# Performance work log

Hardware: AMD Instinct MI355X
Metric: run time of the kernel (lower is better)

The kernel has to match this reference:

```python
import jax, jax.numpy as jnp
import numpy as np

BATCH = 8
IMG = 224
PATCH = 16
IN_CH = 8
D_MODEL = 768
DEPTH = 4
D_INNER = 2 * D_MODEL          # 1536
D_STATE = 16
DT_RANK = D_MODEL // 16        # 48
D_CONV = 4
NUM_CLASSES = 1000
EPS = 1e-5


def setup_inputs() -> dict:
    key = jax.random.key(0)
    ks = jax.random.split(key, 16)
    g = lambda i, shape, s=0.02: jax.random.normal(ks[i], shape, jnp.float32) * s
    L = DEPTH
    inp = {}
    inp['x'] = jax.random.normal(ks[0], (BATCH, IN_CH, IMG, IMG), jnp.float32)
    # patch embed: Conv3d(1, D, (1,p,p)) == shared 2D conv applied to every channel
    inp['patch_w'] = g(1, (D_MODEL, PATCH, PATCH))
    inp['patch_b'] = jnp.zeros((D_MODEL,), jnp.float32)
    inp['channel_embed'] = g(2, (IN_CH, D_MODEL))
    # per-block params (stacked over depth)
    inp['norm_w'] = jnp.ones((L, D_MODEL), jnp.float32)
    inp['norm_b'] = jnp.zeros((L, D_MODEL), jnp.float32)
    inp['in_proj_w'] = g(3, (L, 2 * D_INNER, D_MODEL))
    inp['conv_w'] = g(4, (L, D_INNER, D_CONV), 0.1)
    inp['conv_b'] = jnp.zeros((L, D_INNER), jnp.float32)
    inp['x_proj_w'] = g(5, (L, DT_RANK + 2 * D_STATE, D_INNER))
    inp['dt_proj_w'] = g(6, (L, D_INNER, DT_RANK), 0.1)
    inp['dt_proj_b'] = jnp.full((L, D_INNER), -4.6, jnp.float32)  # softplus^-1(0.01)
    inp['A_log'] = jnp.tile(jnp.log(jnp.arange(1, D_STATE + 1, dtype=jnp.float32)), (L, D_INNER, 1))
    inp['D_param'] = jnp.ones((L, D_INNER), jnp.float32)
    inp['ssm_norm_w'] = jnp.ones((L, D_INNER), jnp.float32)
    inp['ssm_norm_b'] = jnp.zeros((L, D_INNER), jnp.float32)
    inp['out_proj_w'] = g(7, (L, D_MODEL, D_INNER), 0.02 / np.sqrt(L))
    # final norm + classification head
    inp['norm_f_w'] = jnp.ones((D_MODEL,), jnp.float32)
    inp['norm_f_b'] = jnp.zeros((D_MODEL,), jnp.float32)
    inp['head_w'] = g(8, (NUM_CLASSES, D_MODEL))
    inp['head_b'] = jnp.zeros((NUM_CLASSES,), jnp.float32)
    return inp


def _ln(x, w, b):
    mu = x.mean(-1, keepdims=True)
    var = ((x - mu) ** 2).mean(-1, keepdims=True)
    return (x - mu) * jax.lax.rsqrt(var + EPS) * w + b


def _silu(x):
    return x * jax.nn.sigmoid(x)


def _mamba(h, ipw, cw, cb, xpw, dtw, dtb, Alog, Dp, snw, snb, opw):
    # h: [B, L, D_MODEL]
    B, Lseq, _ = h.shape
    xz = jnp.einsum('bld,ed->ble', h, ipw)               # [B, L, 2*di]
    x, z = jnp.split(xz, 2, axis=-1)
    # causal depthwise conv1d along L (kernel D_CONV)
    xp = jnp.pad(x, ((0, 0), (D_CONV - 1, 0), (0, 0)))
    xc = cb + sum(xp[:, k:k + Lseq, :] * cw[:, k] for k in range(D_CONV))
    x = _silu(xc)
    dbc = jnp.einsum('bld,ed->ble', x, xpw)              # [B, L, dt_rank+2N]
    dt_r = dbc[..., :DT_RANK]
    Bm = dbc[..., DT_RANK:DT_RANK + D_STATE]
    Cm = dbc[..., DT_RANK + D_STATE:]
    dt = jax.nn.softplus(jnp.einsum('blr,dr->bld', dt_r, dtw) + dtb)  # [B, L, di]
    A = -jnp.exp(Alog)                                    # [di, N]

    def step(hstate, t):
        dt_t, B_t, C_t, x_t = t                           # [B,di],[B,N],[B,N],[B,di]
        dA = jnp.exp(dt_t[..., None] * A)                 # [B, di, N]
        hstate = dA * hstate + (dt_t * x_t)[..., None] * B_t[:, None, :]
        y = jnp.einsum('bdn,bn->bd', hstate, C_t)
        return hstate, y

    h0 = jnp.zeros((B, D_INNER, D_STATE), x.dtype)
    xs = (dt.transpose(1, 0, 2), Bm.transpose(1, 0, 2),
          Cm.transpose(1, 0, 2), x.transpose(1, 0, 2))
    _, ys = jax.lax.scan(step, h0, xs)                    # [L, B, di]
    y = ys.transpose(1, 0, 2) + Dp * x
    y = _ln(y, snw, snb)                                  # norm-after-SSM
    y = y * _silu(z)
    return jnp.einsum('ble,de->bld', y, opw)


def reference(x, patch_w, patch_b, channel_embed, norm_w, norm_b, in_proj_w,
              conv_w, conv_b, x_proj_w, dt_proj_w, dt_proj_b, A_log, D_param,
              ssm_norm_w, ssm_norm_b, out_proj_w, norm_f_w, norm_f_b,
              head_w, head_b):
    B, C, H, W = x.shape
    hg, wg = H // PATCH, W // PATCH
    # shared-filter patch embed per channel: [B,C,hg,wg,D]
    xp = x.reshape(B, C, hg, PATCH, wg, PATCH)
    emb = jnp.einsum('bchpwq,dpq->bchwd', xp, patch_w) + patch_b
    emb = emb + channel_embed[None, :, None, None, :]
    # Channel-First scan order -> token order (h, w, C): [B, hg*wg*C, D]
    tok = emb.transpose(0, 2, 3, 1, 4).reshape(B, hg * wg * C, D_MODEL)

    hidden, residual = tok, None
    for i in range(DEPTH):
        residual = hidden if residual is None else residual + hidden
        hn = _ln(residual, norm_w[i], norm_b[i])
        hidden = _mamba(hn, in_proj_w[i], conv_w[i], conv_b[i], x_proj_w[i],
                        dt_proj_w[i], dt_proj_b[i], A_log[i], D_param[i],
                        ssm_norm_w[i], ssm_norm_b[i], out_proj_w[i])
    residual = residual + hidden
    hf = _ln(residual, norm_f_w, norm_f_b)
    pooled = hf.mean(axis=1)                              # mean pooling head
    return pooled @ head_w.T + head_b
```

## Files before the change

### kernel.cpp

```cpp
#include <hip/hip_runtime.h>
#include <hip/hip_bf16.h>

typedef __hip_bfloat16 bf16;
typedef __attribute__((ext_vector_type(8))) short short8;
typedef __attribute__((ext_vector_type(4))) float float4v;

#define BATCH 8
#define SEQ   1568
#define M_TOK (BATCH*SEQ)
#define DM    768
#define DI    1536
#define DS    16
#define DTR   48
#define NCLS  1000
#define LAYERS 4
#define CHUNK 112
#define NCH   14

__device__ __forceinline__ float b2f(bf16 v){ return __bfloat162float(v); }
__device__ __forceinline__ bf16  f2b(float v){ return __float2bfloat16(v); }
__device__ __forceinline__ float us2f(unsigned short u){
    unsigned v = ((unsigned)u) << 16; float f; __builtin_memcpy(&f, &v, 4); return f;
}
__device__ __forceinline__ void gload_lds16(const void* g, void* l){
    __builtin_amdgcn_global_load_lds(
        (const __attribute__((address_space(1))) void*)g,
        (__attribute__((address_space(3))) void*)l, 16, 0, 0);
}
template<int CTRL>
__device__ __forceinline__ float dpp_add(float p){
    int pi; __builtin_memcpy(&pi, &p, 4);
    int mi = __builtin_amdgcn_update_dpp(pi, pi, CTRL, 0xF, 0xF, false);
    float m; __builtin_memcpy(&m, &mi, 4);
    return p + m;
}

__global__ void detect_dtype(const unsigned short* __restrict__ probe, unsigned* __restrict__ flag)
{
    if (threadIdx.x == 0 && blockIdx.x == 0) flag[0] = (probe[0] == 0) ? 1u : 0u;
}

__global__ __launch_bounds__(256)
void to_bf16(const unsigned* __restrict__ flag, const void* __restrict__ src,
             bf16* __restrict__ dst, int n)
{
    int i = blockIdx.x*256 + threadIdx.x;
    if (i >= n) return;
    dst[i] = flag[0] ? f2b(((const float*)src)[i]) : ((const bf16*)src)[i];
}

__global__ __launch_bounds__(256)
void to_f32(const unsigned* __restrict__ flag, const void* __restrict__ src,
            float* __restrict__ dst, int n)
{
    int i = blockIdx.x*256 + threadIdx.x;
    if (i >= n) return;
    dst[i] = flag[0] ? ((const float*)src)[i] : b2f(((const bf16*)src)[i]);
}

__global__ __launch_bounds__(256)
void gather_patches(const bf16* __restrict__ x, bf16* __restrict__ Ap, int b0)
{
    size_t idx = (size_t)blockIdx.x*256 + threadIdx.x;
    int i = (int)(idx & 255);
    int m = (int)(idx >> 8);
    int b = b0 + m / SEQ, s = m % SEQ;
    int hw = s >> 3, c = s & 7;
    int h = hw / 14, w = hw % 14;
    int p = i >> 4, q = i & 15;
    Ap[idx] = x[(((size_t)(b*8 + c)*224) + h*16 + p)*224 + w*16 + q];
}

__global__ __launch_bounds__(256)
void gemm_mfma(const bf16* __restrict__ A, int lda,
               const bf16* __restrict__ W, int ldw,
               float* __restrict__ Cf, bf16* __restrict__ Cb, int ldc,
               const float* __restrict__ bias, const float* __restrict__ chan,
               int M, int N, int K, int epi)
{
    __shared__ short As[128*40];
    __shared__ short Bs[128*40];
    int tid  = threadIdx.x;
    int m0   = blockIdx.x*128, n0 = blockIdx.y*128;
    int lane = tid & 63, wv = tid >> 6;
    int wm = (wv >> 1)*64, wn = (wv & 1)*64;
    int l15 = lane & 15, quad = lane >> 4;

    float4v acc[4][4];
    #pragma unroll
    for (int i = 0; i < 4; ++i)
        #pragma unroll
        for (int j = 0; j < 4; ++j) acc[i][j] = (float4v){0.f,0.f,0.f,0.f};

    const short8 zv8 = {0,0,0,0,0,0,0,0};
    for (int k0 = 0; k0 < K; k0 += 32) {
        #pragma unroll
        for (int u = 0; u < 2; ++u) {
            int c   = tid*2 + u;
            int row = c >> 2, ch = c & 3;
            bool kok = (k0 + ch*8 + 8) <= K;
            short8 va = (kok && m0 + row < M)
                ? *(const short8*)((const short*)A + (size_t)(m0+row)*lda + k0 + ch*8) : zv8;
            *(short8*)(As + row*40 + ch*8) = va;
            short8 vb = (kok && n0 + row < N)
                ? *(const short8*)((const short*)W + (size_t)(n0+row)*ldw + k0 + ch*8) : zv8;
            *(short8*)(Bs + row*40 + ch*8) = vb;
        }
        __syncthreads();
        short8 av[4], bv[4];
        #pragma unroll
        for (int i = 0; i < 4; ++i) av[i] = *(const short8*)(As + (wm + i*16 + l15)*40 + quad*8);
        #pragma unroll
        for (int j = 0; j < 4; ++j) bv[j] = *(const short8*)(Bs + (wn + j*16 + l15)*40 + quad*8);
        #pragma unroll
        for (int i = 0; i < 4; ++i)
            #pragma unroll
            for (int j = 0; j < 4; ++j)
                acc[i][j] = __builtin_amdgcn_mfma_f32_16x16x32_bf16(av[i], bv[j], acc[i][j], 0, 0, 0);
        __syncthreads();
    }

    #pragma unroll
    for (int i = 0; i < 4; ++i) {
        #pragma unroll
        for (int j = 0; j < 4; ++j) {
            int gn = n0 + wn + j*16 + l15;
            if (gn >= N) continue;
            #pragma unroll
            for (int r = 0; r < 4; ++r) {
                int gm = m0 + wm + i*16 + quad*4 + r;
                if (gm >= M) continue;
                float v = acc[i][j][r];
                size_t off = (size_t)gm*ldc + gn;
                if (epi == 0)      Cb[off] = f2b(v);
                else if (epi == 1) {
                    v += bias[gn];
                    v = (v > 20.f) ? v : log1pf(__expf(v));
                    Cb[off] = f2b(v);
                }
                else if (epi == 2) Cf[off] += v;
                else               Cf[off] = v + bias[gn] + chan[(size_t)(gm & 7)*N + gn];
            }
        }
    }
}

__global__ __launch_bounds__(256)
void gemm_mfma_fast(const bf16* __restrict__ A, int lda,
                    const bf16* __restrict__ W, int ldw,
                    float* __restrict__ Cf, bf16* __restrict__ Cb, int ldc,
                    const float* __restrict__ bias, const float* __restrict__ chan,
                    int N, int K, int epi)
{
    __shared__ short As[128*32];
    __shared__ short Bs[128*32];
    int tid  = threadIdx.x;
    int m0   = blockIdx.x*128, n0 = blockIdx.y*128;
    int lane = tid & 63, wv = tid >> 6;
    int wm = (wv >> 1)*64, wn = (wv & 1)*64;
    int l15 = lane & 15, quad = lane >> 4;

    int srow = (lane >> 2);
    int skof = (lane & 3) * 8;

    float4v acc[4][4];
    #pragma unroll
    for (int i = 0; i < 4; ++i)
        #pragma unroll
        for (int j = 0; j < 4; ++j) acc[i][j] = (float4v){0.f,0.f,0.f,0.f};

    const short* Ab = (const short*)A;
    const short* Wb = (const short*)W;

    for (int k0 = 0; k0 < K; k0 += 32) {
        #pragma unroll
        for (int u = 0; u < 2; ++u) {
            int c = wv*2 + u;
            int row = c*16 + srow;
            gload_lds16(Ab + (size_t)(m0+row)*lda + k0 + skof, As + c*512);
            gload_lds16(Wb + (size_t)(n0+row)*ldw + k0 + skof, Bs + c*512);
        }
        __syncthreads();
        short8 av[4], bv[4];
        #pragma unroll
        for (int i = 0; i < 4; ++i) av[i] = *(const short8*)(As + (wm + i*16 + l15)*32 + quad*8);
        #pragma unroll
        for (int j = 0; j < 4; ++j) bv[j] = *(const short8*)(Bs + (wn + j*16 + l15)*32 + quad*8);
        #pragma unroll
        for (int i = 0; i < 4; ++i)
            #pragma unroll
            for (int j = 0; j < 4; ++j)
                acc[i][j] = __builtin_amdgcn_mfma_f32_16x16x32_bf16(av[i], bv[j], acc[i][j], 0, 0, 0);
        __syncthreads();
    }

    #pragma unroll
    for (int i = 0; i < 4; ++i) {
        #pragma unroll
        for (int j = 0; j < 4; ++j) {
            int gn = n0 + wn + j*16 + l15;
            #pragma unroll
            for (int r = 0; r < 4; ++r) {
                int gm = m0 + wm + i*16 + quad*4 + r;
                float v = acc[i][j][r];
                size_t off = (size_t)gm*ldc + gn;
                if (epi == 0)      Cb[off] = f2b(v);
                else if (epi == 1) {
                    v += bias[gn];
                    v = (v > 20.f) ? v : log1pf(__expf(v));
                    Cb[off] = f2b(v);
                }
                else if (epi == 2) Cf[off] += v;
                else               Cf[off] = v + bias[gn] + chan[(size_t)(gm & 7)*N + gn];
            }
        }
    }
}

__global__ __launch_bounds__(256)
void ln768(const float* __restrict__ X, const float* __restrict__ w,
           const float* __restrict__ bb, bf16* __restrict__ out)
{
    __shared__ float red[8];
    size_t t = blockIdx.x;
    const float* x = X + t*DM;
    float v[3]; float s = 0.f, s2 = 0.f;
    #pragma unroll
    for (int r = 0; r < 3; ++r) {
        v[r] = x[threadIdx.x + 256*r];
        s += v[r]; s2 += v[r]*v[r];
    }
    #pragma unroll
    for (int o = 32; o; o >>= 1) { s += __shfl_down(s, o, 64); s2 += __shfl_down(s2, o, 64); }
    if ((threadIdx.x & 63) == 0) { red[threadIdx.x >> 6] = s; red[(threadIdx.x >> 6) + 4] = s2; }
    __syncthreads();
    s  = red[0]+red[1]+red[2]+red[3];
    s2 = red[4]+red[5]+red[6]+red[7];
    float mu  = s * (1.f/DM);
    float inv = rsqrtf(fmaxf(s2*(1.f/DM) - mu*mu, 0.f) + 1e-5f);
    #pragma unroll
    for (int r = 0; r < 3; ++r) {
        int i = threadIdx.x + 256*r;
        out[t*DM + i] = f2b((v[r]-mu)*inv*w[i] + bb[i]);
    }
}

__global__ __launch_bounds__(256)
void conv_silu(const bf16* __restrict__ xh, const float* __restrict__ cw,
               const float* __restrict__ cb, bf16* __restrict__ xc)
{
    size_t idx = (size_t)blockIdx.x*256 + threadIdx.x;
    int dv = (int)(idx % (DI/8));
    int m  = (int)(idx / (DI/8));
    int b = m / SEQ, t = m % SEQ;
    int d = dv*8;

    float4v cwq[8];
    #pragma unroll
    for (int j = 0; j < 8; ++j) cwq[j] = *(const float4v*)(cw + (size_t)(d+j)*4);

    float acc[8];
    #pragma unroll
    for (int j = 0; j < 8; ++j) acc[j] = cb[d+j];

    #pragma unroll
    for (int k = 0; k < 4; ++k) {
        int tt = t + k - 3;
        if (tt >= 0) {
            short8 v = *(const short8*)((const short*)xh + (size_t)(b*SEQ + tt)*DI + d);
            #pragma unroll
            for (int j = 0; j < 8; ++j)
                acc[j] += us2f((unsigned short)v[j]) * cwq[j][k];
        }
    }
    short8 o;
    #pragma unroll
    for (int j = 0; j < 8; ++j) {
        float sig = 1.f/(1.f + __expf(-acc[j]));
        bf16 r = f2b(acc[j]*sig);
        unsigned short u; __builtin_memcpy(&u, &r, 2); o[j] = (short)u;
    }
    *(short8*)((short*)xc + idx*8) = o;
}


__global__ __launch_bounds__(256)
void scan_pass1(const bf16* __restrict__ dt, const bf16* __restrict__ x,
                const bf16* __restrict__ dbc, const float* __restrict__ Alog,
                float* __restrict__ hend, float* __restrict__ Pprod, int nin)
{
    __shared__ float dtsT[2][16][20], xsT[2][16][20], BshT[2][16][20];
    int c  = blockIdx.x / nin;
    int r  = blockIdx.x % nin;
    int b  = r / 96;
    int d0 = (r % 96) * 16;
    int tid = threadIdx.x;
    int s  = tid & 15;
    int dl = tid >> 4;
    int d  = d0 + dl;

    float A2 = -__expf(Alog[(size_t)d*DS + s]) * 1.44269504f;
    float h = 0.f, sdt = 0.f;

    int wv   = tid >> 6;
    int lane = tid & 63;
    int st = lane >> 2;
    int sd = (lane & 3) * 4;
    int tbase = c * CHUNK;
    const int NT = CHUNK/16;

    const unsigned short* sp0 = nullptr;
    size_t rstride = 0;
    float* dst0 = nullptr;
    {
        size_t rb = (size_t)(b*SEQ + st);
        if (wv == 0)      { sp0 = (const unsigned short*)dt  + rb*DI + d0 + sd; rstride = DI; dst0 = &dtsT[0][0][0]; }
        else if (wv == 1) { sp0 = (const unsigned short*)x   + rb*DI + d0 + sd; rstride = DI; dst0 = &xsT[0][0][0]; }
        else if (wv == 2) { sp0 = (const unsigned short*)dbc + rb*80 + DTR + sd; rstride = 80; dst0 = &BshT[0][0][0]; }
    }
    const size_t bufstride = 16*20;

    ushort4 vr;
    if (wv < 3) {
        vr = *(const ushort4*)(sp0 + (size_t)tbase*rstride);
        dst0[(sd+0)*20 + st] = us2f(vr.x);
        dst0[(sd+1)*20 + st] = us2f(vr.y);
        dst0[(sd+2)*20 + st] = us2f(vr.z);
        dst0[(sd+3)*20 + st] = us2f(vr.w);
        vr = *(const ushort4*)(sp0 + (size_t)(tbase+16)*rstride);
    }
    __syncthreads();

    for (int t = 0; t < NT; ++t) {
        int cur = t & 1;
        if (wv < 3) {
            if (t+1 < NT) {
                float* dstp = dst0 + (size_t)(cur^1)*bufstride;
                dstp[(sd+0)*20 + st] = us2f(vr.x);
                dstp[(sd+1)*20 + st] = us2f(vr.y);
                dstp[(sd+2)*20 + st] = us2f(vr.z);
                dstp[(sd+3)*20 + st] = us2f(vr.w);
            }
            if (t+2 < NT)
                vr = *(const ushort4*)(sp0 + (size_t)(tbase+(t+2)*16)*rstride);
        }
        #pragma unroll
        for (int jj = 0; jj < 16; jj += 4) {
            float4v dtq = *(const float4v*)&dtsT[cur][dl][jj];
            float4v xq  = *(const float4v*)&xsT [cur][dl][jj];
            float4v Bq  = *(const float4v*)&BshT[cur][s][jj];
            #pragma unroll
            for (int k = 0; k < 4; ++k) {
                float dtv = dtq[k];
                h = exp2f(dtv*A2)*h + (dtv*xq[k])*Bq[k];
                sdt += dtv;
            }
        }
        __syncthreads();
    }
    size_t o = ((size_t)c*nin + r)*256 + tid;
    hend [o] = h;
    Pprod[o] = exp2f(A2*sdt);
}

__global__ __launch_bounds__(256)
void scan_mid(const float* __restrict__ hend, const float* __restrict__ Pprod,
              float* __restrict__ hstart, int nin)
{
    int r = blockIdx.x, tid = threadIdx.x;
    float h = 0.f;
    hstart[(size_t)r*256 + tid] = 0.f;
    for (int c = 1; c < NCH; ++c) {
        size_t p = ((size_t)(c-1)*nin + r)*256 + tid;
        h = Pprod[p]*h + hend[p];
        hstart[((size_t)c*nin + r)*256 + tid] = h;
    }
}

__global__ __launch_bounds__(256)
void scan_pass2(const bf16* __restrict__ dt, const bf16* __restrict__ x,
                const bf16* __restrict__ dbc, const float* __restrict__ Alog,
                const float* __restrict__ Dpar, const float* __restrict__ hstart,
                bf16* __restrict__ y, int nin)
{
    __shared__ float dtsT[2][16][20], xsT[2][16][20], BshT[2][16][20], CshT[2][16][20];
    __shared__ bf16  ys[16][16];
    int c  = blockIdx.x / nin;
    int r  = blockIdx.x % nin;
    int b  = r / 96;
    int d0 = (r % 96) * 16;
    int tid = threadIdx.x;
    int s  = tid & 15;
    int dl = tid >> 4;
    int d  = d0 + dl;

    float A2 = -__expf(Alog[(size_t)d*DS + s]) * 1.44269504f;
    float Dv = Dpar[d];
    float h  = hstart[((size_t)c*nin + r)*256 + tid];

    int wv   = tid >> 6;
    int lane = tid & 63;
    int st = lane >> 2;
    int sd = (lane & 3) * 4;
    int tbase = c * CHUNK;
    const int NT = CHUNK/16;

    const unsigned short* sp0;
    size_t rstride;
    float* dst0;
    {
        size_t rb = (size_t)(b*SEQ + st);
        if (wv == 0)      { sp0 = (const unsigned short*)dt  + rb*DI + d0 + sd;       rstride = DI; dst0 = &dtsT[0][0][0]; }
        else if (wv == 1) { sp0 = (const unsigned short*)x   + rb*DI + d0 + sd;       rstride = DI; dst0 = &xsT[0][0][0]; }
        else if (wv == 2) { sp0 = (const unsigned short*)dbc + rb*80 + DTR + sd;      rstride = 80; dst0 = &BshT[0][0][0]; }
        else              { sp0 = (const unsigned short*)dbc + rb*80 + DTR + DS + sd; rstride = 80; dst0 = &CshT[0][0][0]; }
    }
    const size_t bufstride = 16*20;

    ushort4 vr = *(const ushort4*)(sp0 + (size_t)tbase*rstride);
    dst0[(sd+0)*20 + st] = us2f(vr.x);
    dst0[(sd+1)*20 + st] = us2f(vr.y);
    dst0[(sd+2)*20 + st] = us2f(vr.z);
    dst0[(sd+3)*20 + st] = us2f(vr.w);
    vr = *(const ushort4*)(sp0 + (size_t)(tbase+16)*rstride);
    __syncthreads();

    for (int t = 0; t < NT; ++t) {
        int cur = t & 1;
        if (t+1 < NT) {
            float* dstp = dst0 + (size_t)(cur^1)*bufstride;
            dstp[(sd+0)*20 + st] = us2f(vr.x);
            dstp[(sd+1)*20 + st] = us2f(vr.y);
            dstp[(sd+2)*20 + st] = us2f(vr.z);
            dstp[(sd+3)*20 + st] = us2f(vr.w);
        }
        if (t+2 < NT)
            vr = *(const ushort4*)(sp0 + (size_t)(tbase+(t+2)*16)*rstride);

        #pragma unroll
        for (int jj = 0; jj < 16; jj += 4) {
            float4v dtq = *(const float4v*)&dtsT[cur][dl][jj];
            float4v xq  = *(const float4v*)&xsT [cur][dl][jj];
            float4v Bq  = *(const float4v*)&BshT[cur][s][jj];
            float4v Cq  = *(const float4v*)&CshT[cur][s][jj];
            #pragma unroll
            for (int k = 0; k < 4; ++k) {
                float dtv = dtq[k];
                float xv  = xq[k];
                h = exp2f(dtv*A2)*h + (dtv*xv)*Bq[k];
                float p = h*Cq[k];
                p = dpp_add<0xB1>(p);
                p = dpp_add<0x4E>(p);
                p = dpp_add<0x124>(p);
                p = dpp_add<0x128>(p);
                if (s == 0) ys[jj+k][dl] = f2b(p + Dv*xv);
            }
        }
        __syncthreads();
        if (wv == 0) {
            size_t rowm = (size_t)(b*SEQ + tbase + t*16 + st);
            ushort4 vy = *(const ushort4*)((const unsigned short*)&ys[st][0] + sd);
            *(ushort4*)((unsigned short*)y + rowm*DI + d0 + sd) = vy;
        }
        __syncthreads();
    }
}

__global__ __launch_bounds__(256)
void gate_ln(const bf16* __restrict__ y, const bf16* __restrict__ z,
             const float* __restrict__ w, const float* __restrict__ bb,
             bf16* __restrict__ out)
{
    __shared__ float red[8];
    size_t t = blockIdx.x;
    const bf16* yy = y + t*DI;
    const bf16* zz = z + t*DI;
    float v[6]; float s = 0.f, s2 = 0.f;
    #pragma unroll
    for (int r = 0; r < 6; ++r) {
        v[r] = b2f(yy[threadIdx.x + 256*r]);
        s += v[r]; s2 += v[r]*v[r];
    }
    #pragma unroll
    for (int o = 32; o; o >>= 1) { s += __shfl_down(s, o, 64); s2 += __shfl_down(s2, o, 64); }
    if ((threadIdx.x & 63) == 0) { red[threadIdx.x >> 6] = s; red[(threadIdx.x >> 6) + 4] = s2; }
    __syncthreads();
    s  = red[0]+red[1]+red[2]+red[3];
    s2 = red[4]+red[5]+red[6]+red[7];
    float mu  = s * (1.f/DI);
    float inv = rsqrtf(fmaxf(s2*(1.f/DI) - mu*mu, 0.f) + 1e-5f);
    #pragma unroll
    for (int r = 0; r < 6; ++r) {
        int i = threadIdx.x + 256*r;
        float zv = b2f(zz[i]);
        float sig = 1.f/(1.f + __expf(-zv));
        out[t*DI + i] = f2b(((v[r]-mu)*inv*w[i] + bb[i]) * (zv*sig));
    }
}

__global__ __launch_bounds__(256)
void pool_kernel(const bf16* __restrict__ hf, float* __restrict__ pooled)
{
    int idx = blockIdx.x*256 + threadIdx.x;
    int b = idx / DM, dm = idx % DM;
    const bf16* p = hf + (size_t)b*SEQ*DM + dm;
    float s = 0.f;
    for (int t = 0; t < SEQ; ++t) s += b2f(p[(size_t)t*DM]);
    pooled[idx] = s * (1.f/SEQ);
}

__global__ __launch_bounds__(256)
void head_kernel(const unsigned* __restrict__ flag,
                 const float* __restrict__ pooled, const bf16* __restrict__ hw,
                 const float* __restrict__ hb, void* __restrict__ out)
{
    int idx = blockIdx.x*256 + threadIdx.x;
    if (idx >= BATCH*NCLS) return;
    int b = idx & 7, n = idx >> 3;
    const float* p = pooled + b*DM;
    const unsigned short* w = (const unsigned short*)hw + (size_t)n*DM;
    float acc = hb[n];
    for (int k = 0; k < DM; k += 4) {
        ushort4 wv = *(const ushort4*)(w + k);
        acc += p[k]*us2f(wv.x) + p[k+1]*us2f(wv.y) + p[k+2]*us2f(wv.z) + p[k+3]*us2f(wv.w);
    }
    int o = b*NCLS + n;
    if (flag[0]) ((float*)out)[o] = acc;
    else         ((bf16*)out)[o]  = f2b(acc);
}

extern "C" void kernel_launch(void* const* d_in, const int* in_sizes, int n_in,
                              void* d_out, int out_size, void* d_ws, size_t ws_size,
                              hipStream_t stream)
{
    (void)n_in; (void)out_size;
    dim3 blk(256);

    const bool is_f32[21] = { false, false, true, true, true, true, false, true, true,
                              false, false, true,  true, true, true, true, false,
                              true,  true,  false, true };

    size_t off = 0;
    auto carve = [&](size_t bytes) -> void* {
        void* q = (char*)d_ws + off;
        off += (bytes + 255) & ~(size_t)255;
        return q;
    };

    unsigned* flag = (unsigned*)carve(256);
    void* canon[21];
    for (int i = 0; i < 21; ++i)
        canon[i] = carve((size_t)in_sizes[i] * (is_f32[i] ? 4 : 2));

    float* residual = (float*)carve((size_t)M_TOK*DM*4);
    bf16*  hn       = (bf16*) carve((size_t)M_TOK*DM*2);
    float* pooled   = (float*)carve((size_t)BATCH*DM*4);

    const size_t scanbuf1 = (size_t)NCH*96*256*4;
    const size_t inner1 = 4*(((size_t)SEQ*DI*2 + 255) & ~(size_t)255)
                          + (((size_t)SEQ*80*2 + 255) & ~(size_t)255)
                          + 3*((scanbuf1 + 255) & ~(size_t)255);
    int g = 8;
    while (g > 1 && off + (size_t)g*inner1 > ws_size) g >>= 1;

    bf16* xh  = (bf16*)carve((size_t)g*SEQ*DI*2);
    bf16* zh  = (bf16*)carve((size_t)g*SEQ*DI*2);
    bf16* xc  = (bf16*)carve((size_t)g*SEQ*DI*2);
    bf16* dtb = (bf16*)carve((size_t)g*SEQ*DI*2);
    bf16* dbc = (bf16*)carve((size_t)g*SEQ*80*2);
    float* hend   = (float*)carve((size_t)g*scanbuf1);
    float* Pprod  = (float*)carve((size_t)g*scanbuf1);
    float* hstart = (float*)carve((size_t)g*scanbuf1);
    bf16* Ap    = xh;
    bf16* ybuf  = xh;
    bf16* gated = dtb;

    detect_dtype<<<1, 64, 0, stream>>>((const unsigned short*)d_in[4], flag);
    for (int i = 0; i < 21; ++i) {
        int n = in_sizes[i];
        int gr = (n + 255)/256;
        if (is_f32[i]) to_f32 <<<gr, blk, 0, stream>>>(flag, d_in[i], (float*)canon[i], n);
        else           to_bf16<<<gr, blk, 0, stream>>>(flag, d_in[i], (bf16*) canon[i], n);
    }

    const bf16*  xin   = (const bf16*) canon[0];
    const bf16*  pw    = (const bf16*) canon[1];
    const float* pb    = (const float*)canon[2];
    const float* chan  = (const float*)canon[3];
    const float* nw    = (const float*)canon[4];
    const float* nb    = (const float*)canon[5];
    const bf16*  ipw   = (const bf16*) canon[6];
    const float* cw    = (const float*)canon[7];
    const float* cb    = (const float*)canon[8];
    const bf16*  xpw   = (const bf16*) canon[9];
    const bf16*  dtw   = (const bf16*) canon[10];
    const float* dtbia = (const float*)canon[11];
    const float* Alog  = (const float*)canon[12];
    const float* Dpar  = (const float*)canon[13];
    const float* snw   = (const float*)canon[14];
    const float* snb   = (const float*)canon[15];
    const bf16*  opw   = (const bf16*) canon[16];
    const float* nfw   = (const float*)canon[17];
    const float* nfb   = (const float*)canon[18];
    const bf16*  hw    = (const bf16*) canon[19];
    const float* hb    = (const float*)canon[20];

    const int MG  = g*SEQ;
    const int GXm = (MG + 127)/128;
    const int nin = g*96;

    auto launch_gemm = [&](const bf16* A, int lda, const bf16* W, int ldw,
                           float* Cf, bf16* Cb, int ldc,
                           const float* bias, const float* chan_,
                           int M, int N, int K, int epi) {
        dim3 gr((M + 127)/128, (N + 127)/128);
        if ((M & 127) == 0 && (N & 127) == 0 && (K & 31) == 0)
            gemm_mfma_fast<<<gr, blk, 0, stream>>>(A, lda, W, ldw, Cf, Cb, ldc,
                                                   bias, chan_, N, K, epi);
        else
            gemm_mfma<<<gr, blk, 0, stream>>>(A, lda, W, ldw, Cf, Cb, ldc,
                                              bias, chan_, M, N, K, epi);
    };

    for (int b0 = 0; b0 < BATCH; b0 += g) {
        gather_patches<<<MG, blk, 0, stream>>>(xin, Ap, b0);
        launch_gemm(Ap, 256, pw, 256,
                    residual + (size_t)b0*SEQ*DM, nullptr, DM,
                    pb, chan, MG, DM, 256, 3);
    }

    for (int l = 0; l < LAYERS; ++l) {
        ln768<<<M_TOK, blk, 0, stream>>>(residual, nw + l*DM, nb + l*DM, hn);
        for (int b0 = 0; b0 < BATCH; b0 += g) {
            const bf16* hng = hn + (size_t)b0*SEQ*DM;
            launch_gemm(hng, DM, ipw + (size_t)l*2*DI*DM, DM,
                        nullptr, xh, DI, nullptr, nullptr, MG, DI, DM, 0);
            launch_gemm(hng, DM, ipw + (size_t)l*2*DI*DM + (size_t)DI*DM, DM,
                        nullptr, zh, DI, nullptr, nullptr, MG, DI, DM, 0);
            conv_silu<<<(MG*(DI/8))/256, blk, 0, stream>>>(xh, cw + (size_t)l*DI*4, cb + l*DI, xc);
            launch_gemm(xc, DI, xpw + (size_t)l*80*DI, DI,
                        nullptr, dbc, 80, nullptr, nullptr, MG, 80, DI, 0);
            launch_gemm(dbc, 80, dtw + (size_t)l*DI*DTR, DTR,
                        nullptr, dtb, DI, dtbia + l*DI, nullptr, MG, DI, DTR, 1);
            scan_pass1<<<(NCH-1)*nin, blk, 0, stream>>>(dtb, xc, dbc,
                                                        Alog + (size_t)l*DI*DS,
                                                        hend, Pprod, nin);
            scan_mid<<<nin, blk, 0, stream>>>(hend, Pprod, hstart, nin);
            scan_pass2<<<NCH*nin, blk, 0, stream>>>(dtb, xc, dbc,
                                                    Alog + (size_t)l*DI*DS,
                                                    Dpar + l*DI, hstart, ybuf, nin);
            gate_ln<<<MG, blk, 0, stream>>>(ybuf, zh, snw + l*DI, snb + l*DI, gated);
            launch_gemm(gated, DI, opw + (size_t)l*DM*DI, DI,
                        residual + (size_t)b0*SEQ*DM, nullptr, DM,
                        nullptr, nullptr, MG, DM, DI, 2);
        }
    }

    ln768<<<M_TOK, blk, 0, stream>>>(residual, nfw, nfb, hn);
    pool_kernel<<<(BATCH*DM)/256, blk, 0, stream>>>(hn, pooled);
    head_kernel<<<(BATCH*NCLS + 255)/256, blk, 0, stream>>>(flag, pooled, hw, hb, d_out);
}
```

Measured before the change: 3.957 ms.

## Give each scan thread four states and widen blocks to 64 channels

The selective-scan kernels are remapped so each thread owns four SSM states for one channel instead of one, and each block covers 64 channels instead of 16. dt and x are now loaded once per channel rather than per state, LDS staging is spread across all waves, and the C reduction needs two DPP steps instead of four. The output write uses all threads. This cuts redundant LDS reads and shuffle work per state, in exchange for more registers per thread and a quarter as many blocks.

```diff
diff --git a/kernel.cpp b/kernel.cpp
--- a/kernel.cpp
+++ b/kernel.cpp
@@ -287,93 +287,94 @@
 __global__ __launch_bounds__(256)
 void scan_pass1(const bf16* __restrict__ dt, const bf16* __restrict__ x,
                 const bf16* __restrict__ dbc, const float* __restrict__ Alog,
-                float* __restrict__ hend, float* __restrict__ Pprod, int nin)
-{
-    __shared__ float dtsT[2][16][20], xsT[2][16][20], BshT[2][16][20];
-    int c  = blockIdx.x / nin;
-    int r  = blockIdx.x % nin;
-    int b  = r / 96;
-    int d0 = (r % 96) * 16;
+                float* __restrict__ hend, float* __restrict__ Pprod, int nin2)
+{
+    __shared__ float dtT[2][64][20], xT[2][64][20];
+    __shared__ float BsT[2][16][16];
+    int c  = blockIdx.x / nin2;
+    int r  = blockIdx.x % nin2;
+    int b  = r / 24;
+    int d0 = (r % 24) * 64;
     int tid = threadIdx.x;
-    int s  = tid & 15;
-    int dl = tid >> 4;
+    int sq = tid & 3;
+    int dl = tid >> 2;
     int d  = d0 + dl;
 
-    float A2 = -__expf(Alog[(size_t)d*DS + s]) * 1.44269504f;
-    float h = 0.f, sdt = 0.f;
-
-    int wv   = tid >> 6;
-    int lane = tid & 63;
-    int st = lane >> 2;
-    int sd = (lane & 3) * 4;
+    float4v Aq = *(const float4v*)(Alog + (size_t)d*DS + sq*4);
+    float A2[4], h[4];
+    #pragma unroll
+    for (int k = 0; k < 4; ++k) { A2[k] = -__expf(Aq[k]) * 1.44269504f; h[k] = 0.f; }
+    float sdt = 0.f;
+
+    int js = tid >> 4, dg = tid & 15;
+    bool doB = tid < 64;
+    int j2 = tid >> 2;
+
+    const unsigned short* pdt = (const unsigned short*)dt + ((size_t)b*SEQ + js)*DI + d0 + dg*4;
+    const unsigned short* px  = (const unsigned short*)x  + ((size_t)b*SEQ + js)*DI + d0 + dg*4;
+    const unsigned short* pbc = (const unsigned short*)dbc + ((size_t)b*SEQ + (j2 & 15))*80 + DTR + sq*4;
     int tbase = c * CHUNK;
     const int NT = CHUNK/16;
 
-    const unsigned short* sp0 = nullptr;
-    size_t rstride = 0;
-    float* dst0 = nullptr;
-    {
-        size_t rb = (size_t)(b*SEQ + st);
-        if (wv == 0)      { sp0 = (const unsigned short*)dt  + rb*DI + d0 + sd; rstride = DI; dst0 = &dtsT[0][0][0]; }
-        else if (wv == 1) { sp0 = (const unsigned short*)x   + rb*DI + d0 + sd; rstride = DI; dst0 = &xsT[0][0][0]; }
-        else if (wv == 2) { sp0 = (const unsigned short*)dbc + rb*80 + DTR + sd; rstride = 80; dst0 = &BshT[0][0][0]; }
-    }
-    const size_t bufstride = 16*20;
-
-    ushort4 vr;
-    if (wv < 3) {
-        vr = *(const ushort4*)(sp0 + (size_t)tbase*rstride);
-        dst0[(sd+0)*20 + st] = us2f(vr.x);
-        dst0[(sd+1)*20 + st] = us2f(vr.y);
-        dst0[(sd+2)*20 + st] = us2f(vr.z);
-        dst0[(sd+3)*20 + st] = us2f(vr.w);
-        vr = *(const ushort4*)(sp0 + (size_t)(tbase+16)*rstride);
-    }
+    ushort4 vdt, vx, vbc;
+    auto stage = [&](int buf){
+        dtT[buf][dg*4+0][js] = us2f(vdt.x); dtT[buf][dg*4+1][js] = us2f(vdt.y);
+        dtT[buf][dg*4+2][js] = us2f(vdt.z); dtT[buf][dg*4+3][js] = us2f(vdt.w);
+        xT [buf][dg*4+0][js] = us2f(vx.x);  xT [buf][dg*4+1][js] = us2f(vx.y);
+        xT [buf][dg*4+2][js] = us2f(vx.z);  xT [buf][dg*4+3][js] = us2f(vx.w);
+        if (doB)
+            *(float4v*)&BsT[buf][j2][sq*4] =
+                (float4v){us2f(vbc.x), us2f(vbc.y), us2f(vbc.z), us2f(vbc.w)};
+    };
+    auto fetch = [&](int T){
+        vdt = *(const ushort4*)(pdt + (size_t)(tbase + T*16)*DI);
+        vx  = *(const ushort4*)(px  + (size_t)(tbase + T*16)*DI);
+        if (doB) vbc = *(const ushort4*)(pbc + (size_t)(tbase + T*16)*80);
+    };
+
+    fetch(0); stage(0); fetch(1);
     __syncthreads();
 
     for (int t = 0; t < NT; ++t) {
         int cur = t & 1;
-        if (wv < 3) {
-            if (t+1 < NT) {
-                float* dstp = dst0 + (size_t)(cur^1)*bufstride;
-                dstp[(sd+0)*20 + st] = us2f(vr.x);
-                dstp[(sd+1)*20 + st] = us2f(vr.y);
-                dstp[(sd+2)*20 + st] = us2f(vr.z);
-                dstp[(sd+3)*20 + st] = us2f(vr.w);
-            }
-            if (t+2 < NT)
-                vr = *(const ushort4*)(sp0 + (size_t)(tbase+(t+2)*16)*rstride);
-        }
+        if (t+1 < NT) stage(cur^1);
+        if (t+2 < NT) fetch(t+2);
         #pragma unroll
         for (int jj = 0; jj < 16; jj += 4) {
-            float4v dtq = *(const float4v*)&dtsT[cur][dl][jj];
-            float4v xq  = *(const float4v*)&xsT [cur][dl][jj];
-            float4v Bq  = *(const float4v*)&BshT[cur][s][jj];
+            float4v dtq = *(const float4v*)&dtT[cur][dl][jj];
+            float4v xq  = *(const float4v*)&xT [cur][dl][jj];
             #pragma unroll
-            for (int k = 0; k < 4; ++k) {
-                float dtv = dtq[k];
-                h = exp2f(dtv*A2)*h + (dtv*xq[k])*Bq[k];
+            for (int k2 = 0; k2 < 4; ++k2) {
+                float dtv = dtq[k2];
+                float dtx = dtv * xq[k2];
+                float4v Bq = *(const float4v*)&BsT[cur][jj+k2][sq*4];
+                #pragma unroll
+                for (int k = 0; k < 4; ++k)
+                    h[k] = exp2f(dtv*A2[k])*h[k] + dtx*Bq[k];
                 sdt += dtv;
             }
         }
         __syncthreads();
     }
-    size_t o = ((size_t)c*nin + r)*256 + tid;
-    hend [o] = h;
-    Pprod[o] = exp2f(A2*sdt);
+    size_t o = (((size_t)c*nin2 + r)*256 + tid)*4;
+    *(float4v*)(hend + o) = (float4v){h[0], h[1], h[2], h[3]};
+    *(float4v*)(Pprod + o) = (float4v){exp2f(A2[0]*sdt), exp2f(A2[1]*sdt),
+                                       exp2f(A2[2]*sdt), exp2f(A2[3]*sdt)};
 }
 
 __global__ __launch_bounds__(256)
 void scan_mid(const float* __restrict__ hend, const float* __restrict__ Pprod,
-              float* __restrict__ hstart, int nin)
+              float* __restrict__ hstart, int nin2)
 {
     int r = blockIdx.x, tid = threadIdx.x;
-    float h = 0.f;
-    hstart[(size_t)r*256 + tid] = 0.f;
+    float4v h = (float4v){0.f,0.f,0.f,0.f};
+    *(float4v*)(hstart + ((size_t)r*256 + tid)*4) = h;
     for (int c = 1; c < NCH; ++c) {
-        size_t p = ((size_t)(c-1)*nin + r)*256 + tid;
-        h = Pprod[p]*h + hend[p];
-        hstart[((size_t)c*nin + r)*256 + tid] = h;
+        size_t p = (((size_t)(c-1)*nin2 + r)*256 + tid)*4;
+        float4v P  = *(const float4v*)(Pprod + p);
+        float4v he = *(const float4v*)(hend + p);
+        h = P*h + he;
+        *(float4v*)(hstart + (((size_t)c*nin2 + r)*256 + tid)*4) = h;
     }
 }
 
@@ -381,86 +382,92 @@
 void scan_pass2(const bf16* __restrict__ dt, const bf16* __restrict__ x,
                 const bf16* __restrict__ dbc, const float* __restrict__ Alog,
                 const float* __restrict__ Dpar, const float* __restrict__ hstart,
-                bf16* __restrict__ y, int nin)
-{
-    __shared__ float dtsT[2][16][20], xsT[2][16][20], BshT[2][16][20], CshT[2][16][20];
-    __shared__ bf16  ys[16][16];
-    int c  = blockIdx.x / nin;
-    int r  = blockIdx.x % nin;
-    int b  = r / 96;
-    int d0 = (r % 96) * 16;
+                bf16* __restrict__ y, int nin2)
+{
+    __shared__ float dtT[2][64][20], xT[2][64][20];
+    __shared__ float BsT[2][16][16], CsT[2][16][16];
+    __shared__ bf16  ys[16][64];
+    int c  = blockIdx.x / nin2;
+    int r  = blockIdx.x % nin2;
+    int b  = r / 24;
+    int d0 = (r % 24) * 64;
     int tid = threadIdx.x;
-    int s  = tid & 15;
-    int dl = tid >> 4;
+    int sq = tid & 3;
+    int dl = tid >> 2;
     int d  = d0 + dl;
 
-    float A2 = -__expf(Alog[(size_t)d*DS + s]) * 1.44269504f;
+    float4v Aq = *(const float4v*)(Alog + (size_t)d*DS + sq*4);
+    float A2[4], h[4];
+    {
+        float4v h0 = *(const float4v*)(hstart + (((size_t)c*nin2 + r)*256 + tid)*4);
+        #pragma unroll
+        for (int k = 0; k < 4; ++k) { A2[k] = -__expf(Aq[k]) * 1.44269504f; h[k] = h0[k]; }
+    }
     float Dv = Dpar[d];
-    float h  = hstart[((size_t)c*nin + r)*256 + tid];
-
-    int wv   = tid >> 6;
-    int lane = tid & 63;
-    int st = lane >> 2;
-    int sd = (lane & 3) * 4;
+
+    int js = tid >> 4, dg = tid & 15;
+    bool doBC = tid < 128;
+    int j2 = (tid & 63) >> 2;
+
+    const unsigned short* pdt = (const unsigned short*)dt + ((size_t)b*SEQ + js)*DI + d0 + dg*4;
+    const unsigned short* px  = (const unsigned short*)x  + ((size_t)b*SEQ + js)*DI + d0 + dg*4;
+    const unsigned short* pbc = (const unsigned short*)dbc + ((size_t)b*SEQ + j2)*80 + DTR
+                                + ((tid >= 64) ? DS : 0) + sq*4;
+    float* bc0 = (tid < 64) ? &BsT[0][j2][sq*4] : &CsT[0][j2][sq*4];
     int tbase = c * CHUNK;
     const int NT = CHUNK/16;
 
-    const unsigned short* sp0;
-    size_t rstride;
-    float* dst0;
-    {
-        size_t rb = (size_t)(b*SEQ + st);
-        if (wv == 0)      { sp0 = (const unsigned short*)dt  + rb*DI + d0 + sd;       rstride = DI; dst0 = &dtsT[0][0][0]; }
-        else if (wv == 1) { sp0 = (const unsigned short*)x   + rb*DI + d0 + sd;       rstride = DI; dst0 = &xsT[0][0][0]; }
-        else if (wv == 2) { sp0 = (const unsigned short*)dbc + rb*80 + DTR + sd;      rstride = 80; dst0 = &BshT[0][0][0]; }
-        else              { sp0 = (const unsigned short*)dbc + rb*80 + DTR + DS + sd; rstride = 80; dst0 = &CshT[0][0][0]; }
-    }
-    const size_t bufstride = 16*20;
-
-    ushort4 vr = *(const ushort4*)(sp0 + (size_t)tbase*rstride);
-    dst0[(sd+0)*20 + st] = us2f(vr.x);
-    dst0[(sd+1)*20 + st] = us2f(vr.y);
-    dst0[(sd+2)*20 + st] = us2f(vr.z);
-    dst0[(sd+3)*20 + st] = us2f(vr.w);
-    vr = *(const ushort4*)(sp0 + (size_t)(tbase+16)*rstride);
+    ushort4 vdt, vx, vbc;
+    auto stage = [&](int buf){
+        dtT[buf][dg*4+0][js] = us2f(vdt.x); dtT[buf][dg*4+1][js] = us2f(vdt.y);
+        dtT[buf][dg*4+2][js] = us2f(vdt.z); dtT[buf][dg*4+3][js] = us2f(vdt.w);
+        xT [buf][dg*4+0][js] = us2f(vx.x);  xT [buf][dg*4+1][js] = us2f(vx.y);
+        xT [buf][dg*4+2][js] = us2f(vx.z);  xT [buf][dg*4+3][js] = us2f(vx.w);
+        if (doBC)
+            *(float4v*)(bc0 + (size_t)buf*256) =
+                (float4v){us2f(vbc.x), us2f(vbc.y), us2f(vbc.z), us2f(vbc.w)};
+    };
+    auto fetch = [&](int T){
+        vdt = *(const ushort4*)(pdt + (size_t)(tbase + T*16)*DI);
+        vx  = *(const ushort4*)(px  + (size_t)(tbase + T*16)*DI);
+        if (doBC) vbc = *(const ushort4*)(pbc + (size_t)(tbase + T*16)*80);
+    };
+
+    fetch(0); stage(0); fetch(1);
     __syncthreads();
 
     for (int t = 0; t < NT; ++t) {
         int cur = t & 1;
-        if (t+1 < NT) {
-            float* dstp = dst0 + (size_t)(cur^1)*bufstride;
-            dstp[(sd+0)*20 + st] = us2f(vr.x);
-            dstp[(sd+1)*20 + st] = us2f(vr.y);
-            dstp[(sd+2)*20 + st] = us2f(vr.z);
-            dstp[(sd+3)*20 + st] = us2f(vr.w);
-        }
-        if (t+2 < NT)
-            vr = *(const ushort4*)(sp0 + (size_t)(tbase+(t+2)*16)*rstride);
+        if (t+1 < NT) stage(cur^1);
+        if (t+2 < NT) fetch(t+2);
 
         #pragma unroll
         for (int jj = 0; jj < 16; jj += 4) {
-            float4v dtq = *(const float4v*)&dtsT[cur][dl][jj];
-            float4v xq  = *(const float4v*)&xsT [cur][dl][jj];
-            float4v Bq  = *(const float4v*)&BshT[cur][s][jj];
-            float4v Cq  = *(const float4v*)&CshT[cur][s][jj];
+            float4v dtq = *(const float4v*)&dtT[cur][dl][jj];
+            float4v xq  = *(const float4v*)&xT [cur][dl][jj];
             #pragma unroll
-            for (int k = 0; k < 4; ++k) {
-                float dtv = dtq[k];
-                float xv  = xq[k];
-                h = exp2f(dtv*A2)*h + (dtv*xv)*Bq[k];
-                float p = h*Cq[k];
+            for (int k2 = 0; k2 < 4; ++k2) {
+                float dtv = dtq[k2];
+                float xv  = xq[k2];
+                float dtx = dtv * xv;
+                float4v Bq = *(const float4v*)&BsT[cur][jj+k2][sq*4];
+                float4v Cq = *(const float4v*)&CsT[cur][jj+k2][sq*4];
+                float p = 0.f;
+                #pragma unroll
+                for (int k = 0; k < 4; ++k) {
+                    h[k] = exp2f(dtv*A2[k])*h[k] + dtx*Bq[k];
+                    p += h[k]*Cq[k];
+                }
                 p = dpp_add<0xB1>(p);
                 p = dpp_add<0x4E>(p);
-                p = dpp_add<0x124>(p);
-                p = dpp_add<0x128>(p);
-                if (s == 0) ys[jj+k][dl] = f2b(p + Dv*xv);
+                if (sq == 0) ys[jj+k2][dl] = f2b(p + Dv*xv);
             }
         }
         __syncthreads();
-        if (wv == 0) {
-            size_t rowm = (size_t)(b*SEQ + tbase + t*16 + st);
-            ushort4 vy = *(const ushort4*)((const unsigned short*)&ys[st][0] + sd);
-            *(ushort4*)((unsigned short*)y + rowm*DI + d0 + sd) = vy;
+        {
+            size_t rowm = (size_t)(b*SEQ + tbase + t*16 + js);
+            ushort4 vy = *(const ushort4*)((const unsigned short*)&ys[js][0] + dg*4);
+            *(ushort4*)((unsigned short*)y + rowm*DI + d0 + dg*4) = vy;
         }
         __syncthreads();
     }
@@ -607,7 +614,7 @@
 
     const int MG  = g*SEQ;
     const int GXm = (MG + 127)/128;
-    const int nin = g*96;
+    const int nin2 = g*24;
 
     auto launch_gemm = [&](const bf16* A, int lda, const bf16* W, int ldw,
                            float* Cf, bf16* Cb, int ldc,
@@ -642,13 +649,13 @@
                         nullptr, dbc, 80, nullptr, nullptr, MG, 80, DI, 0);
             launch_gemm(dbc, 80, dtw + (size_t)l*DI*DTR, DTR,
                         nullptr, dtb, DI, dtbia + l*DI, nullptr, MG, DI, DTR, 1);
-            scan_pass1<<<(NCH-1)*nin, blk, 0, stream>>>(dtb, xc, dbc,
-                                                        Alog + (size_t)l*DI*DS,
-                                                        hend, Pprod, nin);
-            scan_mid<<<nin, blk, 0, stream>>>(hend, Pprod, hstart, nin);
-            scan_pass2<<<NCH*nin, blk, 0, stream>>>(dtb, xc, dbc,
-                                                    Alog + (size_t)l*DI*DS,
-                                                    Dpar + l*DI, hstart, ybuf, nin);
+            scan_pass1<<<(NCH-1)*nin2, blk, 0, stream>>>(dtb, xc, dbc,
+                                                         Alog + (size_t)l*DI*DS,
+                                                         hend, Pprod, nin2);
+            scan_mid<<<nin2, blk, 0, stream>>>(hend, Pprod, hstart, nin2);
+            scan_pass2<<<NCH*nin2, blk, 0, stream>>>(dtb, xc, dbc,
+                                                     Alog + (size_t)l*DI*DS,
+                                                     Dpar + l*DI, hstart, ybuf, nin2);
             gate_ln<<<MG, blk, 0, stream>>>(ybuf, zh, snw + l*DI, snb + l*DI, gated);
             launch_gemm(gated, DI, opw + (size_t)l*DM*DI, DI,
                         residual + (size_t)b0*SEQ*DM, nullptr, DM,
```

After: 3.515 ms. 1.13x faster.
